# Kernel tuning notes

Hardware: AMD Instinct MI355X
Metric: run time of the kernel (lower is better)

## Reference

```python
import jax, jax.numpy as jnp
import numpy as np

STRIDE, PAD, DIL = 1, 1, 1


def setup_inputs() -> dict:
    key = jax.random.key(0)
    k1, k2, k3, k4, k5 = jax.random.split(key, 5)
    B, C, W = 16, 256, 4096
    OC, K = 256, 3
    x = jax.random.normal(k1, (B, C, W), jnp.float32)
    weight = jax.random.normal(k2, (OC, C, K), jnp.float32) * 0.05
    offset = jax.random.normal(k3, (B, K, W), jnp.float32)  # offset_groups = 1
    mask = jax.random.uniform(k4, (B, K, W), jnp.float32)   # modulation in [0,1)
    bias = jax.random.normal(k5, (OC,), jnp.float32) * 0.05
    return {"x": x, "weight": weight, "offset": offset, "mask": mask, "bias": bias}


def _deform_conv1d(x, weight, offset, mask, bias):
    B, C, Win = x.shape
    OC, Cg, K = weight.shape
    Wout = offset.shape[-1]
    G = offset.shape[1] // K       # offset groups
    NG = C // Cg                   # weight groups
    Cpg = C // G                   # channels per offset group

    # sampling positions: p[b,g,k,w] = w*stride - pad + k*dil + offset
    base = jnp.arange(Wout, dtype=x.dtype) * STRIDE - PAD      # [Wout]
    kpos = jnp.arange(K, dtype=x.dtype) * DIL                  # [K]
    p = base[None, None, None, :] + kpos[None, None, :, None] \
        + offset.reshape(B, G, K, Wout)                        # [B,G,K,Wout]

    p0f = jnp.floor(p)
    w1 = p - p0f
    w0 = 1.0 - w1
    i0 = p0f.astype(jnp.int32)
    i1 = i0 + 1

    xg = x.reshape(B, G, Cpg, 1, Win)  # broadcastable over kernel axis

    def gather(idx):
        valid = (idx >= 0) & (idx < Win)                        # [B,G,K,Wout]
        idxc = jnp.clip(idx, 0, Win - 1)[:, :, None, :, :]      # [B,G,1,K,Wout]
        v = jnp.take_along_axis(xg, idxc, axis=-1)              # [B,G,Cpg,K,Wout]
        return jnp.where(valid[:, :, None], v, 0.0)

    sampled = gather(i0) * w0[:, :, None] + gather(i1) * w1[:, :, None]
    sampled = sampled * mask.reshape(B, G, 1, K, Wout)          # modulated (v2)

    # grouped contraction
    s = sampled.reshape(B, NG, Cg, K, Wout)                     # [B,NG,Cg,K,Wout]
    wg = weight.reshape(NG, OC // NG, Cg, K)                    # [NG,OCg,Cg,K]
    out = jnp.einsum('bgckw,gock->bgow', s, wg).reshape(B, OC, Wout)
    return out + bias[None, :, None]


def reference(x, weight, offset, mask, bias):
    return _deform_conv1d(x, weight, offset, mask, bias)
```

## Files before the change

### kernel.cpp

```cpp
#include <hip/hip_runtime.h>

#define BATCH 16
#define CCH   256
#define WLEN  4096
#define OCH   256
#define KW    3
#define CK    768
#define WIN   96
#define SLD   200

typedef short bf16x8 __attribute__((ext_vector_type(8)));
typedef float f32x4  __attribute__((ext_vector_type(4)));

__device__ inline short f2bf(float f) {
    union { float f; unsigned u; } v; v.f = f;
    unsigned r = v.u + 0x7FFFu + ((v.u >> 16) & 1u);
    return (short)(r >> 16);
}

__device__ inline void gl_lds16(const void* g, void* l) {
    __builtin_amdgcn_global_load_lds(
        (const __attribute__((address_space(1))) unsigned int*)g,
        (__attribute__((address_space(3))) unsigned int*)l, 16, 0, 0);
}

__global__ void wconv_kernel(const float* __restrict__ w, short* __restrict__ wb) {
    int i = blockIdx.x * 256 + threadIdx.x;
    wb[i] = f2bf(w[i]);
}

__global__ __launch_bounds__(256)
void deform_fused_kernel(const float* __restrict__ x,
                         const short* __restrict__ wb,
                         const float* __restrict__ off,
                         const float* __restrict__ msk,
                         const float* __restrict__ bias,
                         float* __restrict__ out) {
    __shared__ float Win_s[4 * 16 * WIN];
    __shared__ short Sl[64 * SLD];

    const int t      = threadIdx.x;
    const int b      = blockIdx.x >> 6;
    const int wt     = blockIdx.x & 63;
    const int lane   = t & 63;
    const int wv     = t >> 6;
    const int lr     = lane & 15;
    const int lq     = lane >> 4;
    const int wstart = wt * 64 - 16;
    const int wg     = wt * 64 + lane;

    int   li[3];
    float rw0[3], rw1[3];
#pragma unroll
    for (int k = 0; k < 3; ++k) {
        float o  = off[b * (KW * WLEN) + k * WLEN + wg];
        float m  = msk[b * (KW * WLEN) + k * WLEN + wg];
        float p  = (float)(wg - 1 + k) + o;
        float pf = floorf(p);
        float w1 = p - pf;
        int i0 = (int)pf;
        int i1 = i0 + 1;
        bool v0 = (i0 >= 0) & (i0 < WLEN);
        bool v1 = (i1 >= 0) & (i1 < WLEN);
        li[k]  = min(max(i0 - wstart, 0), WIN - 2);
        rw0[k] = v0 ? m * (1.0f - w1) : 0.0f;
        rw1[k] = v1 ? m * w1 : 0.0f;
    }

    const float* xb = x + (size_t)b * CCH * WLEN;
    float* const wbase = &Win_s[wv * 16 * WIN];

    f32x4 acc[4][4];
#pragma unroll
    for (int i = 0; i < 4; ++i)
#pragma unroll
        for (int j = 0; j < 4; ++j)
            acc[i][j] = (f32x4){0.f, 0.f, 0.f, 0.f};

    const int mbase = wv * 64;

    auto stage = [&](int c) {
        const int c0 = c * 64 + wv * 16;
#pragma unroll
        for (int it = 0; it < 6; ++it) {
            int i   = it * 64 + lane;
            int ch  = i / 24;
            int o16 = i - ch * 24;
            int j0  = min(max(wstart + o16 * 4, 0), WLEN - 4);
            gl_lds16(xb + (size_t)(c0 + ch) * WLEN + j0, wbase + it * 256);
        }
    };

    auto gather = [&]() {
        short buf[48];
#pragma unroll
        for (int dc = 0; dc < 16; ++dc) {
            const float* row = wbase + dc * WIN;
#pragma unroll
            for (int k = 0; k < 3; ++k) {
                float v0 = row[li[k]];
                float v1 = row[li[k] + 1];
                buf[dc * 3 + k] = f2bf(rw0[k] * v0 + rw1[k] * v1);
            }
        }
#pragma unroll
        for (int j = 0; j < 6; ++j)
            *reinterpret_cast<bf16x8*>(&Sl[lane * SLD + wv * 48 + j * 8]) =
                *reinterpret_cast<bf16x8*>(&buf[j * 8]);
    };

    auto mfma_chunk = [&](int c) {
#pragma unroll
        for (int ks = 0; ks < 6; ++ks) {
            bf16x8 af[4], bfv[4];
#pragma unroll
            for (int mt = 0; mt < 4; ++mt)
                af[mt] = *reinterpret_cast<const bf16x8*>(
                    wb + (size_t)(mbase + mt * 16 + lr) * CK + c * 192 + ks * 32 + lq * 8);
#pragma unroll
            for (int nt = 0; nt < 4; ++nt)
                bfv[nt] = *reinterpret_cast<const bf16x8*>(
                    &Sl[(nt * 16 + lr) * SLD + ks * 32 + lq * 8]);
#pragma unroll
            for (int mt = 0; mt < 4; ++mt)
#pragma unroll
                for (int nt = 0; nt < 4; ++nt)
                    acc[mt][nt] = __builtin_amdgcn_mfma_f32_16x16x32_bf16(
                        af[mt], bfv[nt], acc[mt][nt], 0, 0, 0);
        }
    };

    stage(0);
    __syncthreads();
    gather();
    __syncthreads();
    for (int c = 0; c < 4; ++c) {
        if (c < 3) stage(c + 1);
        mfma_chunk(c);
        __syncthreads();
        if (c < 3) {
            gather();
            __syncthreads();
        }
    }

    float* ob = out + ((size_t)b * OCH) * WLEN + wt * 64;
#pragma unroll
    for (int mt = 0; mt < 4; ++mt) {
#pragma unroll
        for (int r = 0; r < 4; ++r) {
            int row = mbase + mt * 16 + lq * 4 + r;
            float bv = bias[row];
            float* orow = ob + (size_t)row * WLEN + lr;
#pragma unroll
            for (int nt = 0; nt < 4; ++nt)
                orow[nt * 16] = acc[mt][nt][r] + bv;
        }
    }
}

extern "C" void kernel_launch(void* const* d_in, const int* in_sizes, int n_in,
                              void* d_out, int out_size, void* d_ws, size_t ws_size,
                              hipStream_t stream) {
    const float* x    = (const float*)d_in[0];
    const float* w    = (const float*)d_in[1];
    const float* off  = (const float*)d_in[2];
    const float* msk  = (const float*)d_in[3];
    const float* bias = (const float*)d_in[4];
    float* out = (float*)d_out;
    short* wb  = (short*)d_ws;

    wconv_kernel<<<768, 256, 0, stream>>>(w, wb);
    deform_fused_kernel<<<BATCH * 64, 256, 0, stream>>>(x, wb, off, msk, bias, out);
}
```

Before: 166.7 us.

## Double-buffer deform-conv staging with 8 waves and 32-channel chunks

Doubles the block to 512 threads (8 waves), each owning 32 output channels instead of 64. The 256 input channels are now processed in 8 chunks of 32, with double-buffered LDS for both the raw x window and the sampled bf16 tile. The async global-to-LDS staging of chunk c+2 and the bilinear gather of chunk c+1 now overlap the MFMA work on chunk c, which also drops one barrier per iteration. The aim is to hide load and gather latency and raise wave-level parallelism. The cost is a larger LDS footprint, more blocks competing per CU, and more frequent barriers across 8 waves.

```diff
diff --git a/kernel.cpp b/kernel.cpp
--- a/kernel.cpp
+++ b/kernel.cpp
@@ -7,9 +7,12 @@
 #define KW    3
 #define CK    768
 #define WIN   96
-#define SLD   200
+#define CHUNK 32
+#define NCHUNK 8
+#define SLD   104
 
 typedef short bf16x8 __attribute__((ext_vector_type(8)));
+typedef short bf16x4 __attribute__((ext_vector_type(4)));
 typedef float f32x4  __attribute__((ext_vector_type(4)));
 
 __device__ inline short f2bf(float f) {
@@ -29,15 +32,15 @@
     wb[i] = f2bf(w[i]);
 }
 
-__global__ __launch_bounds__(256)
+__global__ __launch_bounds__(512, 4)
 void deform_fused_kernel(const float* __restrict__ x,
                          const short* __restrict__ wb,
                          const float* __restrict__ off,
                          const float* __restrict__ msk,
                          const float* __restrict__ bias,
                          float* __restrict__ out) {
-    __shared__ float Win_s[4 * 16 * WIN];
-    __shared__ short Sl[64 * SLD];
+    __shared__ float WinS[2][CHUNK * WIN];
+    __shared__ short SlS[2][64 * SLD];
 
     const int t      = threadIdx.x;
     const int b      = blockIdx.x >> 6;
@@ -68,61 +71,62 @@
     }
 
     const float* xb = x + (size_t)b * CCH * WLEN;
-    float* const wbase = &Win_s[wv * 16 * WIN];
 
-    f32x4 acc[4][4];
+    const int sA = t;
+    const int chA = sA / 24, oA = sA - chA * 24;
+    const int jA  = min(max(wstart + oA * 4, 0), WLEN - 4);
+    const int offA = chA * WLEN + jA;
+    const int sB = 512 + t;
+    const int chB = sB / 24, oB = sB - chB * 24;
+    const int jB  = min(max(wstart + oB * 4, 0), WLEN - 4);
+    const int offB = chB * WLEN + jB;
+
+    f32x4 acc[2][4];
 #pragma unroll
-    for (int i = 0; i < 4; ++i)
+    for (int i = 0; i < 2; ++i)
 #pragma unroll
         for (int j = 0; j < 4; ++j)
             acc[i][j] = (f32x4){0.f, 0.f, 0.f, 0.f};
 
-    const int mbase = wv * 64;
-
-    auto stage = [&](int c) {
-        const int c0 = c * 64 + wv * 16;
-#pragma unroll
-        for (int it = 0; it < 6; ++it) {
-            int i   = it * 64 + lane;
-            int ch  = i / 24;
-            int o16 = i - ch * 24;
-            int j0  = min(max(wstart + o16 * 4, 0), WLEN - 4);
-            gl_lds16(xb + (size_t)(c0 + ch) * WLEN + j0, wbase + it * 256);
-        }
+    auto stage = [&](int c, int bufsel) {
+        const float* src = xb + (size_t)c * CHUNK * WLEN;
+        gl_lds16(src + offA, &WinS[bufsel][wv * 256]);
+        if (wv < 4) gl_lds16(src + offB, &WinS[bufsel][2048 + wv * 256]);
     };
 
-    auto gather = [&]() {
-        short buf[48];
+    auto gather = [&](int bufsel) {
+        short obuf[12];
 #pragma unroll
-        for (int dc = 0; dc < 16; ++dc) {
-            const float* row = wbase + dc * WIN;
+        for (int dc = 0; dc < 4; ++dc) {
+            const float* row = &WinS[bufsel][(wv * 4 + dc) * WIN];
 #pragma unroll
             for (int k = 0; k < 3; ++k) {
                 float v0 = row[li[k]];
                 float v1 = row[li[k] + 1];
-                buf[dc * 3 + k] = f2bf(rw0[k] * v0 + rw1[k] * v1);
+                obuf[dc * 3 + k] = f2bf(rw0[k] * v0 + rw1[k] * v1);
             }
         }
+        short* sp = &SlS[bufsel][lane * SLD + wv * 12];
 #pragma unroll
-        for (int j = 0; j < 6; ++j)
-            *reinterpret_cast<bf16x8*>(&Sl[lane * SLD + wv * 48 + j * 8]) =
-                *reinterpret_cast<bf16x8*>(&buf[j * 8]);
+        for (int j = 0; j < 3; ++j)
+            *reinterpret_cast<bf16x4*>(sp + j * 4) =
+                *reinterpret_cast<const bf16x4*>(&obuf[j * 4]);
     };
 
-    auto mfma_chunk = [&](int c) {
+    auto mfma_chunk = [&](int c, int bufsel) {
 #pragma unroll
-        for (int ks = 0; ks < 6; ++ks) {
-            bf16x8 af[4], bfv[4];
+        for (int ks = 0; ks < 3; ++ks) {
+            bf16x8 af[2], bfv[4];
 #pragma unroll
-            for (int mt = 0; mt < 4; ++mt)
+            for (int mt = 0; mt < 2; ++mt)
                 af[mt] = *reinterpret_cast<const bf16x8*>(
-                    wb + (size_t)(mbase + mt * 16 + lr) * CK + c * 192 + ks * 32 + lq * 8);
+                    wb + (size_t)(wv * 32 + mt * 16 + lr) * CK + c * 96 + ks * 32 + lq * 8);
 #pragma unroll
             for (int nt = 0; nt < 4; ++nt)
                 bfv[nt] = *reinterpret_cast<const bf16x8*>(
-                    &Sl[(nt * 16 + lr) * SLD + ks * 32 + lq * 8]);
+                    &SlS[bufsel][(nt * 16 + lr) * SLD + ks * 32 + lq * 8]);
 #pragma unroll
-            for (int mt = 0; mt < 4; ++mt)
+            for (int mt = 0; mt < 2; ++mt)
 #pragma unroll
                 for (int nt = 0; nt < 4; ++nt)
                     acc[mt][nt] = __builtin_amdgcn_mfma_f32_16x16x32_bf16(
@@ -130,26 +134,26 @@
         }
     };
 
-    stage(0);
+    stage(0, 0);
     __syncthreads();
-    gather();
+    stage(1, 1);
+    gather(0);
     __syncthreads();
-    for (int c = 0; c < 4; ++c) {
-        if (c < 3) stage(c + 1);
-        mfma_chunk(c);
-        __syncthreads();
-        if (c < 3) {
-            gather();
-            __syncthreads();
-        }
+
+#pragma unroll 2
+    for (int c = 0; c < NCHUNK; ++c) {
+        if (c < NCHUNK - 2) stage(c + 2, c & 1);
+        if (c < NCHUNK - 1) gather((c + 1) & 1);
+        mfma_chunk(c, c & 1);
+        if (c < NCHUNK - 1) __syncthreads();
     }
 
     float* ob = out + ((size_t)b * OCH) * WLEN + wt * 64;
 #pragma unroll
-    for (int mt = 0; mt < 4; ++mt) {
+    for (int mt = 0; mt < 2; ++mt) {
 #pragma unroll
         for (int r = 0; r < 4; ++r) {
-            int row = mbase + mt * 16 + lq * 4 + r;
+            int row = wv * 32 + mt * 16 + lq * 4 + r;
             float bv = bias[row];
             float* orow = ob + (size_t)row * WLEN + lr;
 #pragma unroll
@@ -171,5 +175,5 @@
     short* wb  = (short*)d_ws;
 
     wconv_kernel<<<768, 256, 0, stream>>>(w, wb);
-    deform_fused_kernel<<<BATCH * 64, 256, 0, stream>>>(x, wb, off, msk, bias, out);
+    deform_fused_kernel<<<BATCH * 64, 512, 0, stream>>>(x, wb, off, msk, bias, out);
 }
```

Measured after the change: 163.9 us. Within noise of the previous version (-1.7%).
